# Kernel tuning notes

Measured on AMD Instinct MI355X. Metric: run time of the kernel, lower is better.

The kernel has to match this reference:

```python
import jax, jax.numpy as jnp
import numpy as np

N_ATOMS = 100_000
N_EDGES = 1_600_000
N_RADIAL = 16
N_ELEM = 119          # periodic table size used by per-element scale/shift
HIDDEN = 512
N_FEAT = N_RADIAL + N_RADIAL * N_RADIAL  # M0 + M1-contraction features = 272
R_CUT = 5.0
EPS = 1e-8


def setup_inputs() -> dict:
    key = jax.random.key(0)
    ks = jax.random.split(key, 10)
    R = jax.random.normal(ks[0], (N_ATOMS, 3), jnp.float32)
    Z = jax.random.randint(ks[1], (N_ATOMS,), 0, N_ELEM).astype(jnp.int32)
    idx = jax.random.randint(ks[2], (2, N_EDGES), 0, N_ATOMS)
    box = jnp.zeros((3, 3), jnp.float32)
    offsets = jnp.zeros((N_EDGES, 3), jnp.float32)
    # descriptor params: Gaussian radial basis centers / width
    centers = jnp.linspace(0.0, R_CUT, N_RADIAL, dtype=jnp.float32)
    width = jnp.asarray(0.5, jnp.float32)
    # readout MLP params
    W1 = jax.random.normal(ks[3], (N_FEAT, HIDDEN), jnp.float32) / np.sqrt(N_FEAT)
    b1 = jnp.zeros((HIDDEN,), jnp.float32)
    W2 = jax.random.normal(ks[4], (HIDDEN, HIDDEN), jnp.float32) / np.sqrt(HIDDEN)
    b2 = jnp.zeros((HIDDEN,), jnp.float32)
    W3 = jax.random.normal(ks[5], (HIDDEN, 1), jnp.float32) / np.sqrt(HIDDEN)
    b3 = jnp.zeros((1,), jnp.float32)
    # per-element scale/shift
    scale = jnp.ones((N_ELEM,), jnp.float32)
    shift = jax.random.normal(ks[6], (N_ELEM,), jnp.float32)
    return {"R": R, "Z": Z, "idx": idx, "box": box, "offsets": offsets,
            "centers": centers, "width": width,
            "W1": W1, "b1": b1, "W2": W2, "b2": b2, "W3": W3, "b3": b3,
            "scale": scale, "shift": shift}


def reference(R, Z, idx, box, offsets, centers, width,
              W1, b1, W2, b2, W3, b3, scale, shift):
    n = R.shape[0]
    idx_i, idx_j = idx[0], idx[1]
    # edge gather + free displacement (init_box == 0): dr = displacement(Rj, Ri) = Rj - Ri
    dr = R[idx_j] - R[idx_i]                      # (E, 3)
    r = jnp.linalg.norm(dr, axis=-1, keepdims=True)  # (E, 1)
    d = dr / (r + EPS)                            # unit directions (E, 3)
    # Gaussian radial basis (E, K)
    b = jnp.exp(-((r - centers[None, :]) ** 2) / (2.0 * width * width))
    # scatter-sum moments per atom
    M0 = jax.ops.segment_sum(b, idx_i, num_segments=n)                       # (N, K)
    M1 = jax.ops.segment_sum(b[:, :, None] * d[:, None, :], idx_i,
                             num_segments=n)                                 # (N, K, 3)
    # rotation-invariant gaussian-moment contraction
    G1 = jnp.einsum('nad,nbd->nab', M1, M1).reshape(n, -1)                   # (N, K*K)
    feat = jnp.concatenate([M0, G1], axis=-1)                                # (N, 272)
    # per-atom readout MLP (swish)
    h = jax.nn.silu(feat @ W1 + b1)
    h = jax.nn.silu(h @ W2 + b2)
    h = h @ W3 + b3                                                          # (N, 1)
    # per-element scale/shift, then total energy
    atomic_energies = scale[Z][:, None] * h + shift[Z][:, None]
    return jnp.sum(atomic_energies)
```

## Files before the change

kernel.cpp:

```cpp
#include <hip/hip_runtime.h>
#include <hip/hip_bf16.h>
#include <cstdint>

#define HID 512
#define K1P 288
#define K1F 160
#define NBG 96

typedef __attribute__((ext_vector_type(8))) short bf16x8;
typedef __attribute__((ext_vector_type(4))) float f32x4;

__device__ __forceinline__ short f2bf(float x) {
    __hip_bfloat16 h = __float2bfloat16(x);
    return *(short*)&h;
}
__device__ __forceinline__ float silu(float x) {
    return x * (1.0f / (1.0f + __expf(-x)));
}
__device__ __forceinline__ void gl_lds16(const void* src, void* dst) {
    __builtin_amdgcn_global_load_lds(
        (const __attribute__((address_space(1))) void*)src,
        (__attribute__((address_space(3))) void*)dst, 16, 0, 0);
}
__device__ __forceinline__ int xcd_swz(int bid, int nwg) {
    int q = nwg >> 3, r = nwg & 7;
    int xcd = bid & 7, i = bid >> 3;
    int base = (xcd < r) ? xcd * (q + 1) : r * (q + 1) + (xcd - r) * q;
    return base + i;
}
__device__ __forceinline__ void tri_ab(int g, int& a, int& b) {
    int aa = 0, rem = g;
    while (rem >= 16 - aa) { rem -= 16 - aa; ++aa; }
    a = aa; b = aa + rem;
}

__global__ __launch_bounds__(256) void hist_kernel(
    const int* __restrict__ idx, int* __restrict__ counts, int nEdges)
{
    int e = blockIdx.x * 256 + threadIdx.x;
    if (e < nEdges) atomicAdd(&counts[idx[e]], 1);
}

__global__ __launch_bounds__(1024) void scan1_kernel(
    const int* __restrict__ counts, int* __restrict__ starts,
    int* __restrict__ blockSum, int n)
{
    __shared__ int wsum[16];
    int t = threadIdx.x, lane = t & 63, wid = t >> 6;
    int i = blockIdx.x * 1024 + t;
    int v = (i < n) ? counts[i] : 0;
    int incl = v;
    #pragma unroll
    for (int off = 1; off < 64; off <<= 1) {
        int u = __shfl_up(incl, off);
        if (lane >= off) incl += u;
    }
    if (lane == 63) wsum[wid] = incl;
    __syncthreads();
    if (t < 16) {
        int s = wsum[t];
        #pragma unroll
        for (int off = 1; off < 16; off <<= 1) {
            int u = __shfl_up(s, off);
            if (t >= off) s += u;
        }
        wsum[t] = s;
    }
    __syncthreads();
    int woff = (wid == 0) ? 0 : wsum[wid - 1];
    if (i < n) starts[i] = woff + incl - v;
    if (t == 0) blockSum[blockIdx.x] = wsum[15];
}

__global__ __launch_bounds__(1024) void scan2_kernel(
    const int* __restrict__ blockSum, int* __restrict__ blockOff,
    int* __restrict__ starts, int nb, int n)
{
    __shared__ int arr[1024];
    int t = threadIdx.x;
    int v = (t < nb) ? blockSum[t] : 0;
    arr[t] = v;
    __syncthreads();
    #pragma unroll
    for (int off = 1; off < 1024; off <<= 1) {
        int x = (t >= off) ? arr[t - off] : 0;
        __syncthreads();
        arr[t] += x;
        __syncthreads();
    }
    if (t < nb) blockOff[t] = arr[t] - v;
    if (t == 0) starts[n] = arr[nb - 1];
}

__global__ __launch_bounds__(1024) void scan3_kernel(
    int* __restrict__ starts, int* __restrict__ cursor,
    const int* __restrict__ blockOff, int n)
{
    int i = blockIdx.x * 1024 + threadIdx.x;
    if (i < n) {
        int s = starts[i] + blockOff[blockIdx.x];
        starts[i] = s;
        cursor[i] = s;
    }
}

__global__ __launch_bounds__(256) void scatter2_kernel(
    const float* __restrict__ R, const int* __restrict__ idx,
    int* __restrict__ cursor, float4* __restrict__ sorted, int nEdges, int nAtoms)
{
    int g  = blockIdx.x & 7;
    int gb = blockIdx.x >> 3;
    int per = (nAtoms + 7) >> 3;
    int lo = g * per;
    int hi = lo + per; if (hi > nAtoms) hi = nAtoms;

    auto emit = [&](int i, int j) {
        if (i < lo || i >= hi) return;
        float rix = R[3*(size_t)i], riy = R[3*(size_t)i+1], riz = R[3*(size_t)i+2];
        float rjx = R[3*(size_t)j], rjy = R[3*(size_t)j+1], rjz = R[3*(size_t)j+2];
        float dx = rjx - rix, dy = rjy - riy, dz = rjz - riz;
        float r = sqrtf(dx*dx + dy*dy + dz*dz);
        float inv = 1.0f / (r + 1e-8f);
        int pos = atomicAdd(&cursor[i], 1);
        sorted[pos] = make_float4(r, dx*inv, dy*inv, dz*inv);
    };

    if ((nEdges & 3) == 0) {
        int nq = nEdges >> 2;
        const int4* i4p = (const int4*)idx;
        const int4* j4p = (const int4*)(idx + nEdges);
        for (int q = gb * 256 + threadIdx.x; q < nq; q += NBG * 256) {
            int4 iv = i4p[q], jv = j4p[q];
            emit(iv.x, jv.x); emit(iv.y, jv.y);
            emit(iv.z, jv.z); emit(iv.w, jv.w);
        }
    } else {
        for (int e = gb * 256 + threadIdx.x; e < nEdges; e += NBG * 256)
            emit(idx[e], idx[nEdges + e]);
    }
}

__global__ __launch_bounds__(256) void accum_kernel(
    const float4* __restrict__ sorted, const int* __restrict__ starts,
    const float* __restrict__ centers, const float* __restrict__ width,
    float* __restrict__ M0M1, short* __restrict__ feat16,
    int nAtoms, int useFeat)
{
    __shared__ float sm[4][64];
    int wv = threadIdx.x >> 6, lane = threadIdx.x & 63;
    int atom = blockIdx.x * 4 + wv;
    if (atom >= nAtoms) return;
    int s = starts[atom], e = starts[atom + 1];
    int k = lane >> 2, c = lane & 3;
    float ck = centers[k];
    float w = width[0];
    float inv2w2 = 1.0f / (2.0f * w * w);
    float acc = 0.0f;
    auto term = [&](float4 v) {
        float diff = v.x - ck;
        float b = __expf(-diff * diff * inv2w2);
        float comp = (c == 0) ? 1.0f : ((c == 1) ? v.y : ((c == 2) ? v.z : v.w));
        return b * comp;
    };
    int p = s;
    for (; p + 3 < e; p += 4) {
        float4 v0 = sorted[p];
        float4 v1 = sorted[p + 1];
        float4 v2 = sorted[p + 2];
        float4 v3 = sorted[p + 3];
        acc += term(v0); acc += term(v1); acc += term(v2); acc += term(v3);
    }
    for (; p < e; ++p) acc += term(sorted[p]);

    if (!useFeat) {
        M0M1[(size_t)atom * 64 + lane] = acc;
        return;
    }
    sm[wv][lane] = acc;
    asm volatile("s_waitcnt lgkmcnt(0)" ::: "memory");
    short* frow = feat16 + (size_t)atom * K1F;
    #pragma unroll
    for (int q = 0; q < 3; ++q) {
        int idx5 = q * 64 + lane;
        if (idx5 >= K1F) break;
        float val;
        if (idx5 < 16) {
            val = sm[wv][4 * idx5];
        } else if (idx5 < 152) {
            int a, b;
            tri_ab(idx5 - 16, a, b);
            val = sm[wv][4*a+1] * sm[wv][4*b+1]
                + sm[wv][4*a+2] * sm[wv][4*b+2]
                + sm[wv][4*a+3] * sm[wv][4*b+3];
        } else {
            val = 0.0f;
        }
        frow[idx5] = f2bf(val);
    }
}

__global__ __launch_bounds__(256) void convW_kernel(
    const float* __restrict__ W, short* __restrict__ Wt, int K, int Kpad, int N)
{
    int n = blockIdx.x * 256 + threadIdx.x;
    int k = blockIdx.y;
    if (n >= N) return;
    float v = (k < K) ? W[(size_t)k * N + n] : 0.0f;
    Wt[(size_t)n * Kpad + k] = f2bf(v);
}

__global__ __launch_bounds__(256) void convW1f_kernel(
    const float* __restrict__ W, short* __restrict__ Wf, int N)
{
    int n = blockIdx.x * 256 + threadIdx.x;
    int k = blockIdx.y;
    if (n >= N) return;
    float v;
    if (k < 16) {
        v = W[(size_t)k * N + n];
    } else if (k < 152) {
        int a, b;
        tri_ab(k - 16, a, b);
        v = W[(size_t)(16 + a*16 + b) * N + n];
        if (b > a) v += W[(size_t)(16 + b*16 + a) * N + n];
    } else {
        v = 0.0f;
    }
    Wf[(size_t)n * K1F + k] = f2bf(v);
}

__global__ __launch_bounds__(256, 2) void gemm1_mfma(
    const float* __restrict__ M0M1, const short* __restrict__ W1t,
    const float* __restrict__ bias, short* __restrict__ C, int M, int nwg)
{
    __shared__ float MsT[64][128];
    __shared__ short Asl[2][4096];
    __shared__ short Bsl[4][4096];
    int t = threadIdx.x;
    int w = t >> 6, lane = t & 63;
    int wr = w >> 1, wc = w & 1;
    int li = lane & 15, lg = lane >> 4;
    int lin = xcd_swz(blockIdx.x, nwg);
    int row0 = (lin >> 2) * 128;
    int col0 = (lin & 3) * 128;

    {
        int mrow = t >> 1, mo = (t & 1) * 32;
        int gm = row0 + mrow; if (gm > M - 1) gm = M - 1;
        const float4* src = (const float4*)(M0M1 + (size_t)gm * 64 + mo);
        #pragma unroll
        for (int q = 0; q < 8; ++q) {
            float4 v = src[q];
            int c0 = mo + q * 4;
            MsT[c0+0][mrow] = v.x; MsT[c0+1][mrow] = v.y;
            MsT[c0+2][mrow] = v.z; MsT[c0+3][mrow] = v.w;
        }
    }
    __syncthreads();

    auto stageA = [&](int kt, int buf) {
        #pragma unroll
        for (int p = 0; p < 2; ++p) {
            int cell = p * 256 + t;
            int k8 = cell >> 7, row = cell & 127;
            int kbase = kt * 32 + k8 * 8;
            bf16x8 v;
            if (kbase < 16) {
                #pragma unroll
                for (int j = 0; j < 8; ++j) v[j] = f2bf(MsT[4*(kbase+j)][row]);
            } else if (kbase < 272) {
                int g = kbase - 16, a = g >> 4, b0 = g & 15;
                float ax = MsT[4*a+1][row], ay = MsT[4*a+2][row], az = MsT[4*a+3][row];
                #pragma unroll
                for (int j = 0; j < 8; ++j) {
                    int b = b0 + j;
                    v[j] = f2bf(ax*MsT[4*b+1][row] + ay*MsT[4*b+2][row] + az*MsT[4*b+3][row]);
                }
            } else {
                #pragma unroll
                for (int j = 0; j < 8; ++j) v[j] = 0;
            }
            *(bf16x8*)&Asl[buf][cell * 8] = v;
        }
    };
    auto stageB = [&](int kt, int buf) {
        #pragma unroll
        for (int p = 0; p < 2; ++p) {
            int cell = p * 256 + t;
            int k8 = cell >> 7, col = cell & 127;
            const short* src = W1t + (size_t)(col0 + col) * K1P + kt*32 + k8*8;
            gl_lds16(src, &Bsl[buf][(p * 256 + w * 64) * 8]);
        }
    };

    f32x4 acc[4][4] = {};
    const int NS = K1P / 32;
    stageA(0, 0);
    stageB(0, 0); stageB(1, 1); stageB(2, 2);

    #pragma unroll
    for (int s = 0; s < NS; ++s) {
        if (s <= NS - 3)      asm volatile("s_waitcnt vmcnt(4) lgkmcnt(0)\n\ts_barrier" ::: "memory");
        else if (s == NS - 2) asm volatile("s_waitcnt vmcnt(2) lgkmcnt(0)\n\ts_barrier" ::: "memory");
        else                  asm volatile("s_waitcnt vmcnt(0) lgkmcnt(0)\n\ts_barrier" ::: "memory");
        if (s + 3 < NS) stageB(s + 3, (s + 3) & 3);
        bf16x8 af[4], bfr[4];
        #pragma unroll
        for (int m = 0; m < 4; ++m)
            af[m] = *(const bf16x8*)&Asl[s & 1][(lg*128 + wr*64 + m*16 + li) * 8];
        #pragma unroll
        for (int n = 0; n < 4; ++n)
            bfr[n] = *(const bf16x8*)&Bsl[s & 3][(lg*128 + wc*64 + n*16 + li) * 8];
        if (s + 1 < NS) stageA(s + 1, (s + 1) & 1);
        __builtin_amdgcn_s_setprio(1);
        #pragma unroll
        for (int m = 0; m < 4; ++m)
            #pragma unroll
            for (int n = 0; n < 4; ++n)
                acc[m][n] = __builtin_amdgcn_mfma_f32_16x16x32_bf16(af[m], bfr[n], acc[m][n], 0, 0, 0);
        __builtin_amdgcn_s_setprio(0);
    }

    float bv[4];
    #pragma unroll
    for (int n = 0; n < 4; ++n) bv[n] = bias[col0 + wc*64 + n*16 + li];
    #pragma unroll
    for (int m = 0; m < 4; ++m)
        #pragma unroll
        for (int r = 0; r < 4; ++r) {
            int row = row0 + wr*64 + m*16 + lg*4 + r;
            if (row >= M) continue;
            size_t base = (size_t)row * HID + col0 + wc*64 + li;
            #pragma unroll
            for (int n = 0; n < 4; ++n) {
                float cx = acc[m][n][r] + bv[n];
                C[base + n*16] = f2bf(silu(cx));
            }
        }
}

__global__ __launch_bounds__(256, 3) void gemm_feat(
    const short* __restrict__ F, const short* __restrict__ W1f,
    const float* __restrict__ bias, short* __restrict__ C, int M, int nwg)
{
    __shared__ short Asl[3][4096];
    __shared__ short Bsl[3][4096];
    int t = threadIdx.x;
    int w = t >> 6, lane = t & 63;
    int wr = w >> 1, wc = w & 1;
    int li = lane & 15, lg = lane >> 4;
    int lin = xcd_swz(blockIdx.x, nwg);
    int row0 = (lin >> 2) * 128;
    int col0 = (lin & 3) * 128;

    int rr = t & 127, k8h = t >> 7;
    int grA = row0 + rr; if (grA > M - 1) grA = M - 1;
    const short* aSrc0 = F + (size_t)grA * K1F + k8h * 8;
    const short* aSrc1 = aSrc0 + 16;
    const short* bSrc0 = W1f + (size_t)(col0 + rr) * K1F + k8h * 8;
    const short* bSrc1 = bSrc0 + 16;

    auto stage = [&](int kt, int buf) {
        gl_lds16(aSrc0 + kt * 32, &Asl[buf][(w * 64) * 8]);
        gl_lds16(aSrc1 + kt * 32, &Asl[buf][(256 + w * 64) * 8]);
        gl_lds16(bSrc0 + kt * 32, &Bsl[buf][(w * 64) * 8]);
        gl_lds16(bSrc1 + kt * 32, &Bsl[buf][(256 + w * 64) * 8]);
    };

    f32x4 acc[4][4] = {};
    const int NS = K1F / 32;
    stage(0, 0); stage(1, 1);

    #pragma unroll
    for (int s = 0; s < NS; ++s) {
        if (s < NS - 1) asm volatile("s_waitcnt vmcnt(4)\n\ts_barrier" ::: "memory");
        else            asm volatile("s_waitcnt vmcnt(0)\n\ts_barrier" ::: "memory");
        if (s + 2 < NS) stage(s + 2, (s + 2) % 3);
        bf16x8 af[4], bfr[4];
        #pragma unroll
        for (int m = 0; m < 4; ++m)
            af[m] = *(const bf16x8*)&Asl[s % 3][(lg*128 + wr*64 + m*16 + li) * 8];
        #pragma unroll
        for (int n = 0; n < 4; ++n)
            bfr[n] = *(const bf16x8*)&Bsl[s % 3][(lg*128 + wc*64 + n*16 + li) * 8];
        __builtin_amdgcn_s_setprio(1);
        #pragma unroll
        for (int m = 0; m < 4; ++m)
            #pragma unroll
            for (int n = 0; n < 4; ++n)
                acc[m][n] = __builtin_amdgcn_mfma_f32_16x16x32_bf16(af[m], bfr[n], acc[m][n], 0, 0, 0);
        __builtin_amdgcn_s_setprio(0);
    }

    float bv[4];
    #pragma unroll
    for (int n = 0; n < 4; ++n) bv[n] = bias[col0 + wc*64 + n*16 + li];
    #pragma unroll
    for (int m = 0; m < 4; ++m)
        #pragma unroll
        for (int r = 0; r < 4; ++r) {
            int row = row0 + wr*64 + m*16 + lg*4 + r;
            if (row >= M) continue;
            size_t base = (size_t)row * HID + col0 + wc*64 + li;
            #pragma unroll
            for (int n = 0; n < 4; ++n) {
                float cx = acc[m][n][r] + bv[n];
                C[base + n*16] = f2bf(silu(cx));
            }
        }
}

__global__ __launch_bounds__(256, 3) void gemm2_mfma(
    const short* __restrict__ A, const short* __restrict__ W2t,
    const float* __restrict__ bias, const float* __restrict__ W3,
    const float* __restrict__ b3, const float* __restrict__ scale,
    const float* __restrict__ shift, const int* __restrict__ Z,
    float* __restrict__ out, int M, int nwg)
{
    __shared__ short Asl[3][4096];
    __shared__ short Bsl[3][4096];
    __shared__ float rsum[2][128];
    __shared__ float red[4];
    int t = threadIdx.x;
    int w = t >> 6, lane = t & 63;
    int wr = w >> 1, wc = w & 1;
    int li = lane & 15, lg = lane >> 4;
    int lin = xcd_swz(blockIdx.x, nwg);
    int row0 = (lin >> 2) * 128;
    int col0 = (lin & 3) * 128;

    int rr = t & 127, k8h = t >> 7;
    int grA = row0 + rr; if (grA > M - 1) grA = M - 1;
    const short* aSrc0 = A + (size_t)grA * HID + k8h * 8;
    const short* aSrc1 = aSrc0 + 16;
    const short* bSrc0 = W2t + (size_t)(col0 + rr) * HID + k8h * 8;
    const short* bSrc1 = bSrc0 + 16;

    auto stage = [&](int kt, int buf) {
        gl_lds16(aSrc0 + kt * 32, &Asl[buf][(w * 64) * 8]);
        gl_lds16(aSrc1 + kt * 32, &Asl[buf][(256 + w * 64) * 8]);
        gl_lds16(bSrc0 + kt * 32, &Bsl[buf][(w * 64) * 8]);
        gl_lds16(bSrc1 + kt * 32, &Bsl[buf][(256 + w * 64) * 8]);
    };

    f32x4 acc[4][4] = {};
    const int NS = HID / 32;
    stage(0, 0); stage(1, 1);

    for (int s = 0; s < NS; ++s) {
        if (s < NS - 1) asm volatile("s_waitcnt vmcnt(4)\n\ts_barrier" ::: "memory");
        else            asm volatile("s_waitcnt vmcnt(0)\n\ts_barrier" ::: "memory");
        if (s + 2 < NS) stage(s + 2, (s + 2) % 3);
        bf16x8 af[4], bfr[4];
        #pragma unroll
        for (int m = 0; m < 4; ++m)
            af[m] = *(const bf16x8*)&Asl[s % 3][(lg*128 + wr*64 + m*16 + li) * 8];
        #pragma unroll
        for (int n = 0; n < 4; ++n)
            bfr[n] = *(const bf16x8*)&Bsl[s % 3][(lg*128 + wc*64 + n*16 + li) * 8];
        __builtin_amdgcn_s_setprio(1);
        #pragma unroll
        for (int m = 0; m < 4; ++m)
            #pragma unroll
            for (int n = 0; n < 4; ++n)
                acc[m][n] = __builtin_amdgcn_mfma_f32_16x16x32_bf16(af[m], bfr[n], acc[m][n], 0, 0, 0);
        __builtin_amdgcn_s_setprio(0);
    }

    float bv[4], w3v[4];
    #pragma unroll
    for (int n = 0; n < 4; ++n) {
        int col = col0 + wc*64 + n*16 + li;
        bv[n]  = bias[col];
        w3v[n] = W3[col];
    }
    #pragma unroll
    for (int m = 0; m < 4; ++m)
        #pragma unroll
        for (int r = 0; r < 4; ++r) {
            float s = 0.f;
            #pragma unroll
            for (int n = 0; n < 4; ++n) {
                float cx = acc[m][n][r] + bv[n];
                s += silu(cx) * w3v[n];
            }
            #pragma unroll
            for (int off = 1; off < 16; off <<= 1) s += __shfl_xor(s, off);
            if (li == 0) rsum[wc][wr*64 + m*16 + lg*4 + r] = s;
        }
    __syncthreads();
    float e = 0.f;
    if (t < 128) {
        int row = row0 + t;
        if (row < M) {
            float v = rsum[0][t] + rsum[1][t];
            int z = Z[row];
            e = scale[z] * v;
            if ((lin & 3) == 0) e += scale[z] * b3[0] + shift[z];
        }
    }
    #pragma unroll
    for (int off = 32; off > 0; off >>= 1) e += __shfl_down(e, off);
    if (lane == 0) red[w] = e;
    __syncthreads();
    if (t == 0) atomicAdd(out, red[0] + red[1] + red[2] + red[3]);
}

extern "C" void kernel_launch(void* const* d_in, const int* in_sizes, int n_in,
                              void* d_out, int out_size, void* d_ws, size_t ws_size,
                              hipStream_t stream)
{
    const float* R       = (const float*)d_in[0];
    const int*   Z       = (const int*)  d_in[1];
    const int*   idx     = (const int*)  d_in[2];
    const float* centers = (const float*)d_in[5];
    const float* width   = (const float*)d_in[6];
    const float* W1      = (const float*)d_in[7];
    const float* b1      = (const float*)d_in[8];
    const float* W2      = (const float*)d_in[9];
    const float* b2      = (const float*)d_in[10];
    const float* W3      = (const float*)d_in[11];
    const float* b3      = (const float*)d_in[12];
    const float* scale   = (const float*)d_in[13];
    const float* shift   = (const float*)d_in[14];

    int nAtoms = in_sizes[0] / 3;
    int nEdges = in_sizes[2] / 2;

    size_t m0m1_b = (size_t)nAtoms * 64 * sizeof(float);
    size_t h1_b   = (size_t)nAtoms * HID * 2;
    size_t w1t_b  = (size_t)HID * K1P * 2;
    size_t w2t_b  = (size_t)HID * HID * 2;
    size_t w1f_b  = (size_t)HID * K1F * 2;
    size_t feat_b = (size_t)nAtoms * K1F * 2;
    if (ws_size < m0m1_b + h1_b + w1t_b + w2t_b) return;
    int useFeat = (ws_size >= m0m1_b + h1_b + w1t_b + w2t_b + w1f_b + feat_b) ? 1 : 0;

    char* ws = (char*)d_ws;
    float* M0M1  = (float*)ws;
    char*  regB  = ws + m0m1_b;
    short* h1    = (short*)regB;
    short* W1t   = (short*)(ws + m0m1_b + h1_b);
    short* W2t   = W1t + (size_t)HID * K1P;
    short* W1f   = W2t + (size_t)HID * HID;
    short* feat16 = (short*)(ws + m0m1_b + h1_b + w1t_b + w2t_b + w1f_b);

    int nb = (nAtoms + 1023) / 1024;
    size_t sorted_b = (size_t)nEdges * sizeof(float4);
    float4* sorted = (float4*)regB;
    int* counts   = (int*)(regB + sorted_b);
    int* starts   = counts + nAtoms;
    int* cursor   = starts + nAtoms + 1;
    int* blockSum = cursor + nAtoms;
    int* blockOff = blockSum + nb;
    if (sorted_b + (size_t)(3 * nAtoms + 1 + 2 * nb) * sizeof(int) > h1_b) return;

    float* out = (float*)d_out;

    hipMemsetAsync(counts, 0, (size_t)nAtoms * sizeof(int), stream);
    hipMemsetAsync(out, 0, sizeof(float), stream);

    convW_kernel<<<dim3(2, K1P), 256, 0, stream>>>(W1, W1t, 272, K1P, HID);
    convW_kernel<<<dim3(2, HID), 256, 0, stream>>>(W2, W2t, HID, HID, HID);
    if (useFeat)
        convW1f_kernel<<<dim3(2, K1F), 256, 0, stream>>>(W1, W1f, HID);

    int eb = (nEdges + 255) / 256;
    hist_kernel <<<eb, 256, 0, stream>>>(idx, counts, nEdges);
    scan1_kernel<<<nb, 1024, 0, stream>>>(counts, starts, blockSum, nAtoms);
    scan2_kernel<<<1, 1024, 0, stream>>>(blockSum, blockOff, starts, nb, nAtoms);
    scan3_kernel<<<nb, 1024, 0, stream>>>(starts, cursor, blockOff, nAtoms);
    scatter2_kernel<<<8 * NBG, 256, 0, stream>>>(R, idx, cursor, sorted, nEdges, nAtoms);
    accum_kernel<<<(nAtoms + 3) / 4, 256, 0, stream>>>(sorted, starts, centers, width,
                                                       M0M1, feat16, nAtoms, useFeat);

    int gb = (nAtoms + 127) / 128;
    int nwg = gb * 4;
    if (useFeat)
        gemm_feat<<<nwg, 256, 0, stream>>>(feat16, W1f, b1, h1, nAtoms, nwg);
    else
        gemm1_mfma<<<nwg, 256, 0, stream>>>(M0M1, W1t, b1, h1, nAtoms, nwg);
    gemm2_mfma<<<nwg, 256, 0, stream>>>(h1, W2t, b2, W3, b3, scale, shift, Z, out, nAtoms, nwg);
}
```

Baseline: 423.3 us.

## Run second MLP layer in FP8 MFMA and vectorize edge histogram

The first-layer GEMM now writes its activations as FP8, and a new FP8 version of the second GEMM uses 16x16x32 fp8 MFMA. W2 is pre-scaled by 16 into FP8 and the accumulator is rescaled by 1/16 afterwards. This halves the bytes moved for h1 and W2 and uses the higher FP8 MFMA rate, at the cost of a large loss of precision in the energy sum. Separately, the histogram kernel loads edge indices as int4 and does four atomics per thread.

```diff
diff --git a/kernel.cpp b/kernel.cpp
--- a/kernel.cpp
+++ b/kernel.cpp
@@ -13,6 +13,10 @@
 __device__ __forceinline__ short f2bf(float x) {
     __hip_bfloat16 h = __float2bfloat16(x);
     return *(short*)&h;
+}
+__device__ __forceinline__ unsigned char f2fp8(float x) {
+    int p = __builtin_amdgcn_cvt_pk_fp8_f32(x, x, 0, false);
+    return (unsigned char)(p & 0xff);
 }
 __device__ __forceinline__ float silu(float x) {
     return x * (1.0f / (1.0f + __expf(-x)));
@@ -35,10 +39,19 @@
 }
 
 __global__ __launch_bounds__(256) void hist_kernel(
-    const int* __restrict__ idx, int* __restrict__ counts, int nEdges)
-{
-    int e = blockIdx.x * 256 + threadIdx.x;
-    if (e < nEdges) atomicAdd(&counts[idx[e]], 1);
+    const int* __restrict__ idx, int* __restrict__ counts, int nEdges, int vec4)
+{
+    int q = blockIdx.x * 256 + threadIdx.x;
+    if (vec4) {
+        int nq = nEdges >> 2;
+        if (q < nq) {
+            int4 v = ((const int4*)idx)[q];
+            atomicAdd(&counts[v.x], 1); atomicAdd(&counts[v.y], 1);
+            atomicAdd(&counts[v.z], 1); atomicAdd(&counts[v.w], 1);
+        }
+    } else {
+        if (q < nEdges) atomicAdd(&counts[idx[q]], 1);
+    }
 }
 
 __global__ __launch_bounds__(1024) void scan1_kernel(
@@ -229,6 +242,15 @@
     Wf[(size_t)n * K1F + k] = f2bf(v);
 }
 
+__global__ __launch_bounds__(256) void convW2f8_kernel(
+    const float* __restrict__ W, unsigned char* __restrict__ Wf, int N)
+{
+    int n = blockIdx.x * 256 + threadIdx.x;
+    int k = blockIdx.y;
+    if (n >= N) return;
+    Wf[(size_t)n * HID + k] = f2fp8(W[(size_t)k * N + n] * 16.0f);
+}
+
 __global__ __launch_bounds__(256, 2) void gemm1_mfma(
     const float* __restrict__ M0M1, const short* __restrict__ W1t,
     const float* __restrict__ bias, short* __restrict__ C, int M, int nwg)
@@ -341,7 +363,7 @@
 
 __global__ __launch_bounds__(256, 3) void gemm_feat(
     const short* __restrict__ F, const short* __restrict__ W1f,
-    const float* __restrict__ bias, short* __restrict__ C, int M, int nwg)
+    const float* __restrict__ bias, unsigned char* __restrict__ C, int M, int nwg)
 {
     __shared__ short Asl[3][4096];
     __shared__ short Bsl[3][4096];
@@ -405,9 +427,101 @@
             #pragma unroll
             for (int n = 0; n < 4; ++n) {
                 float cx = acc[m][n][r] + bv[n];
-                C[base + n*16] = f2bf(silu(cx));
+                C[base + n*16] = f2fp8(silu(cx));
             }
         }
+}
+
+__global__ __launch_bounds__(256, 3) void gemm2_fp8(
+    const unsigned char* __restrict__ A, const unsigned char* __restrict__ W2f,
+    const float* __restrict__ bias, const float* __restrict__ W3,
+    const float* __restrict__ b3, const float* __restrict__ scale,
+    const float* __restrict__ shift, const int* __restrict__ Z,
+    float* __restrict__ out, int M, int nwg)
+{
+    __shared__ __align__(16) unsigned char Asl[3][4096];
+    __shared__ __align__(16) unsigned char Bsl[3][4096];
+    __shared__ float rsum[2][128];
+    __shared__ float red[4];
+    int t = threadIdx.x;
+    int w = t >> 6, lane = t & 63;
+    int wr = w >> 1, wc = w & 1;
+    int li = lane & 15, lg = lane >> 4;
+    int lin = xcd_swz(blockIdx.x, nwg);
+    int row0 = (lin >> 2) * 128;
+    int col0 = (lin & 3) * 128;
+
+    int rr = t & 127, k16 = t >> 7;
+    int grA = row0 + rr; if (grA > M - 1) grA = M - 1;
+    const unsigned char* aSrc = A + (size_t)grA * HID + k16 * 16;
+    const unsigned char* bSrc = W2f + (size_t)(col0 + rr) * HID + k16 * 16;
+
+    auto stage = [&](int kt, int buf) {
+        gl_lds16(aSrc + kt * 32, &Asl[buf][w * 1024]);
+        gl_lds16(bSrc + kt * 32, &Bsl[buf][w * 1024]);
+    };
+
+    f32x4 acc[4][4] = {};
+    const int NS = HID / 32;
+    stage(0, 0); stage(1, 1);
+
+    for (int s = 0; s < NS; ++s) {
+        if (s < NS - 1) asm volatile("s_waitcnt vmcnt(2)\n\ts_barrier" ::: "memory");
+        else            asm volatile("s_waitcnt vmcnt(0)\n\ts_barrier" ::: "memory");
+        if (s + 2 < NS) stage(s + 2, (s + 2) % 3);
+        long af[4], bfr[4];
+        const unsigned char* Ab = &Asl[s % 3][(lg >> 1) * 2048 + (lg & 1) * 8 + (wr*64 + li) * 16];
+        const unsigned char* Bb = &Bsl[s % 3][(lg >> 1) * 2048 + (lg & 1) * 8 + (wc*64 + li) * 16];
+        #pragma unroll
+        for (int m = 0; m < 4; ++m) af[m] = *(const long*)(Ab + m * 256);
+        #pragma unroll
+        for (int n = 0; n < 4; ++n) bfr[n] = *(const long*)(Bb + n * 256);
+        __builtin_amdgcn_s_setprio(1);
+        #pragma unroll
+        for (int m = 0; m < 4; ++m)
+            #pragma unroll
+            for (int n = 0; n < 4; ++n)
+                acc[m][n] = __builtin_amdgcn_mfma_f32_16x16x32_fp8_fp8(af[m], bfr[n], acc[m][n], 0, 0, 0);
+        __builtin_amdgcn_s_setprio(0);
+    }
+
+    float bv[4], w3v[4];
+    #pragma unroll
+    for (int n = 0; n < 4; ++n) {
+        int col = col0 + wc*64 + n*16 + li;
+        bv[n]  = bias[col];
+        w3v[n] = W3[col];
+    }
+    #pragma unroll
+    for (int m = 0; m < 4; ++m)
+        #pragma unroll
+        for (int r = 0; r < 4; ++r) {
+            float s = 0.f;
+            #pragma unroll
+            for (int n = 0; n < 4; ++n) {
+                float cx = acc[m][n][r] * 0.0625f + bv[n];
+                s += silu(cx) * w3v[n];
+            }
+            #pragma unroll
+            for (int off = 1; off < 16; off <<= 1) s += __shfl_xor(s, off);
+            if (li == 0) rsum[wc][wr*64 + m*16 + lg*4 + r] = s;
+        }
+    __syncthreads();
+    float e = 0.f;
+    if (t < 128) {
+        int row = row0 + t;
+        if (row < M) {
+            float v = rsum[0][t] + rsum[1][t];
+            int z = Z[row];
+            e = scale[z] * v;
+            if ((lin & 3) == 0) e += scale[z] * b3[0] + shift[z];
+        }
+    }
+    #pragma unroll
+    for (int off = 32; off > 0; off >>= 1) e += __shfl_down(e, off);
+    if (lane == 0) red[w] = e;
+    __syncthreads();
+    if (t == 0) atomicAdd(out, red[0] + red[1] + red[2] + red[3]);
 }
 
 __global__ __launch_bounds__(256, 3) void gemm2_mfma(
@@ -532,18 +646,21 @@
     size_t w1t_b  = (size_t)HID * K1P * 2;
     size_t w2t_b  = (size_t)HID * HID * 2;
     size_t w1f_b  = (size_t)HID * K1F * 2;
+    size_t w2f8_b = (size_t)HID * HID;
     size_t feat_b = (size_t)nAtoms * K1F * 2;
     if (ws_size < m0m1_b + h1_b + w1t_b + w2t_b) return;
-    int useFeat = (ws_size >= m0m1_b + h1_b + w1t_b + w2t_b + w1f_b + feat_b) ? 1 : 0;
+    int useFeat = (ws_size >= m0m1_b + h1_b + w1t_b + w2t_b + w1f_b + w2f8_b + feat_b) ? 1 : 0;
 
     char* ws = (char*)d_ws;
     float* M0M1  = (float*)ws;
     char*  regB  = ws + m0m1_b;
     short* h1    = (short*)regB;
+    unsigned char* h1f8 = (unsigned char*)regB;
     short* W1t   = (short*)(ws + m0m1_b + h1_b);
     short* W2t   = W1t + (size_t)HID * K1P;
     short* W1f   = W2t + (size_t)HID * HID;
-    short* feat16 = (short*)(ws + m0m1_b + h1_b + w1t_b + w2t_b + w1f_b);
+    unsigned char* W2f8 = (unsigned char*)(W1f + (size_t)HID * K1F);
+    short* feat16 = (short*)(ws + m0m1_b + h1_b + w1t_b + w2t_b + w1f_b + w2f8_b);
 
     int nb = (nAtoms + 1023) / 1024;
     size_t sorted_b = (size_t)nEdges * sizeof(float4);
@@ -561,12 +678,16 @@
     hipMemsetAsync(out, 0, sizeof(float), stream);
 
     convW_kernel<<<dim3(2, K1P), 256, 0, stream>>>(W1, W1t, 272, K1P, HID);
-    convW_kernel<<<dim3(2, HID), 256, 0, stream>>>(W2, W2t, HID, HID, HID);
-    if (useFeat)
+    if (useFeat) {
         convW1f_kernel<<<dim3(2, K1F), 256, 0, stream>>>(W1, W1f, HID);
-
-    int eb = (nEdges + 255) / 256;
-    hist_kernel <<<eb, 256, 0, stream>>>(idx, counts, nEdges);
+        convW2f8_kernel<<<dim3(2, HID), 256, 0, stream>>>(W2, W2f8, HID);
+    } else {
+        convW_kernel<<<dim3(2, HID), 256, 0, stream>>>(W2, W2t, HID, HID, HID);
+    }
+
+    int vec4 = ((nEdges & 3) == 0) ? 1 : 0;
+    int hb = vec4 ? ((nEdges / 4) + 255) / 256 : (nEdges + 255) / 256;
+    hist_kernel <<<hb, 256, 0, stream>>>(idx, counts, nEdges, vec4);
     scan1_kernel<<<nb, 1024, 0, stream>>>(counts, starts, blockSum, nAtoms);
     scan2_kernel<<<1, 1024, 0, stream>>>(blockSum, blockOff, starts, nb, nAtoms);
     scan3_kernel<<<nb, 1024, 0, stream>>>(starts, cursor, blockOff, nAtoms);
@@ -576,9 +697,11 @@
 
     int gb = (nAtoms + 127) / 128;
     int nwg = gb * 4;
-    if (useFeat)
-        gemm_feat<<<nwg, 256, 0, stream>>>(feat16, W1f, b1, h1, nAtoms, nwg);
-    else
+    if (useFeat) {
+        gemm_feat<<<nwg, 256, 0, stream>>>(feat16, W1f, b1, h1f8, nAtoms, nwg);
+        gemm2_fp8<<<nwg, 256, 0, stream>>>(h1f8, W2f8, b2, W3, b3, scale, shift, Z, out, nAtoms, nwg);
+    } else {
         gemm1_mfma<<<nwg, 256, 0, stream>>>(M0M1, W1t, b1, h1, nAtoms, nwg);
-    gemm2_mfma<<<nwg, 256, 0, stream>>>(h1, W2t, b2, W3, b3, scale, shift, Z, out, nAtoms, nwg);
-}
+        gemm2_mfma<<<nwg, 256, 0, stream>>>(h1, W2t, b2, W3, b3, scale, shift, Z, out, nAtoms, nwg);
+    }
+}
```

Result: faster. 408.3 us (-3.5%).
